# Kernel optimization log

Measured on AMD Instinct MI355X. Metric: run time of the kernel, lower is better.

Reference implementation:

```python
import jax, jax.numpy as jnp
from jax import lax
import numpy as np

N_QUBITS = 8
N_LAYERS = 7
DIM = 2 ** N_QUBITS  # 256 amplitudes


def _conv(x, w, b, stride, pad):
    y = lax.conv_general_dilated(x, w, (stride, stride), [(pad, pad), (pad, pad)],
                                 dimension_numbers=("NCHW", "OIHW", "NCHW"))
    return y + b[None, :, None, None]


def _adaptive_pool2(x):
    # AdaptiveAvgPool2d(2) on 7x7 input: bins [0:4) and [3:7) per spatial dim (overlap at idx 3)
    bins = [(0, 4), (3, 7)]
    rows = [x[:, :, s:e, :].mean(axis=2) for s, e in bins]  # each (B,C,7)
    return jnp.stack([jnp.stack([r[:, :, s:e].mean(axis=2) for s, e in bins], axis=-1)
                      for r in rows], axis=-2)  # (B,C,2,2)


def _qsim(feat, weights):
    # Batched 8-qubit statevector simulation. PennyLane default.qubit ordering:
    # wire 0 is the most-significant axis. RY and CNOT are real matrices and the
    # amplitude-embedded state is real, so the state stays real throughout.
    norm = jnp.linalg.norm(feat, axis=1, keepdims=True)
    state = feat / jnp.maximum(norm, 1e-12)  # AmplitudeEmbedding(normalize=True), (B,256)
    B = state.shape[0]
    for layer in range(N_LAYERS):
        for q in range(N_QUBITS):  # RY(weights[layer,q]) on wire q
            theta = weights[layer, q]
            c, s = jnp.cos(theta / 2), jnp.sin(theta / 2)
            st = state.reshape(B, 2 ** q, 2, 2 ** (N_QUBITS - 1 - q))
            s0, s1 = st[:, :, 0, :], st[:, :, 1, :]
            state = jnp.stack([c * s0 - s * s1, s * s0 + c * s1], axis=2).reshape(B, DIM)
        for q in range(N_QUBITS - 1):  # CNOT(control=q, target=q+1)
            st = state.reshape(B, 2 ** q, 2, 2, 2 ** (N_QUBITS - 2 - q))
            swapped = st[:, :, 1, ::-1, :]  # flip target where control=1
            state = jnp.stack([st[:, :, 0], swapped], axis=2).reshape(B, DIM)
    st = state.reshape(B, 2, DIM // 2)
    return jnp.sum(st[:, 0] ** 2, axis=1) - jnp.sum(st[:, 1] ** 2, axis=1)  # <Z_0>


def setup_inputs() -> dict:
    key = jax.random.key(0)
    ks = jax.random.split(key, 24)
    B = 65536
    f32 = jnp.float32
    def nrm(k, shape, scale):
        return jax.random.normal(k, shape, f32) * scale
    return {
        "x": jax.random.normal(ks[0], (B, 1, 28, 28), f32),
        "conv1_w": nrm(ks[1], (3, 1, 5, 5), 0.2), "conv1_b": nrm(ks[2], (3,), 0.1),
        "conv2_w": nrm(ks[3], (6, 3, 3, 3), 0.2), "conv2_b": nrm(ks[4], (6,), 0.1),
        "conv3_w": nrm(ks[5], (12, 6, 3, 3), 0.2), "conv3_b": nrm(ks[6], (12,), 0.1),
        "fc_w": nrm(ks[7], (256, 48), 0.15), "fc_b": nrm(ks[8], (256,), 0.1),
        "q_weights": jax.random.uniform(ks[9], (N_LAYERS, N_QUBITS), f32, 0.0, 2.0 * np.pi),
        "cls1_w": nrm(ks[10], (180, 1), 0.5), "cls1_b": nrm(ks[11], (180,), 0.1),
        "cls2_w": nrm(ks[12], (140, 180), 0.08), "cls2_b": nrm(ks[13], (140,), 0.1),
        "cls3_w": nrm(ks[14], (100, 140), 0.09), "cls3_b": nrm(ks[15], (100,), 0.1),
        "cls4_w": nrm(ks[16], (50, 100), 0.1), "cls4_b": nrm(ks[17], (50,), 0.1),
        "cls5_w": nrm(ks[18], (1, 50), 0.15), "cls5_b": nrm(ks[19], (1,), 0.1),
    }


def reference(x, conv1_w, conv1_b, conv2_w, conv2_b, conv3_w, conv3_b, fc_w, fc_b,
              q_weights, cls1_w, cls1_b, cls2_w, cls2_b, cls3_w, cls3_b,
              cls4_w, cls4_b, cls5_w, cls5_b):
    h = jax.nn.relu(_conv(x, conv1_w, conv1_b, 2, 2))   # (B,3,14,14)
    h = jax.nn.relu(_conv(h, conv2_w, conv2_b, 2, 1))   # (B,6,7,7)
    h = jax.nn.relu(_conv(h, conv3_w, conv3_b, 1, 1))   # (B,12,7,7)
    h = _adaptive_pool2(h).reshape(h.shape[0], -1)      # (B,48)
    feat = jax.nn.relu(h @ fc_w.T + fc_b)               # (B,256); dropout = identity (eval)
    feat = feat / jnp.maximum(jnp.linalg.norm(feat, axis=1, keepdims=True), 1e-12)  # F.normalize
    qout = _qsim(feat, q_weights)[:, None]              # (B,1)
    h = jax.nn.relu(qout @ cls1_w.T + cls1_b)
    h = jax.nn.relu(h @ cls2_w.T + cls2_b)
    h = jax.nn.relu(h @ cls3_w.T + cls3_b)
    h = jax.nn.relu(h @ cls4_w.T + cls4_b)
    return jax.nn.sigmoid(h @ cls5_w.T + cls5_b)        # (B,1)
```

## Files before the change

### kernel.cpp

```cpp
#include <hip/hip_runtime.h>
#include <math.h>


#define WR2_SZ 1664
#define NL   16384

constexpr int QM[7][8] = {
 {0x80,0x40,0x20,0x10,0x08,0x04,0x02,0x01},
 {0xC0,0x60,0x30,0x18,0x0C,0x06,0x03,0x01},
 {0xA0,0x50,0x28,0x14,0x0A,0x05,0x02,0x01},
 {0xF0,0x78,0x3C,0x1E,0x0F,0x07,0x03,0x01},
 {0x88,0x44,0x22,0x11,0x08,0x04,0x02,0x01},
 {0xCC,0x66,0x33,0x19,0x0C,0x06,0x03,0x01},
 {0xAA,0x55,0x2A,0x15,0x0A,0x05,0x02,0x01}};
constexpr int QR[7][8] = {
 {0x80,0x40,0x20,0x10,0x08,0x04,0x02,0x01},
 {0x80,0xC0,0xE0,0xF0,0xF8,0xFC,0xFE,0xFF},
 {0x80,0x40,0xA0,0x50,0xA8,0x54,0xAA,0x55},
 {0x80,0xC0,0x60,0x30,0x98,0xCC,0x66,0x33},
 {0x80,0x40,0x20,0x10,0x88,0x44,0x22,0x11},
 {0x80,0xC0,0xE0,0xF0,0x78,0x3C,0x1E,0x0F},
 {0x80,0x40,0xA0,0x50,0x28,0x14,0x0A,0x05}};

#define ROTSTEP2(L, Q) { \
    constexpr int m_  = QM[L][Q]; \
    constexpr int r_  = QR[L][Q]; \
    constexpr int lm_ = m_ >> 2, rm_ = m_ & 3; \
    constexpr int rl_ = r_ >> 2, rr_ = r_ & 3; \
    constexpr float f1_ = (rr_ & 1) ? -1.f : 1.f; \
    constexpr float f2_ = (rr_ & 2) ? -1.f : 1.f; \
    constexpr float f3_ = f1_ * f2_; \
    const float c_ = qtc[(L) * 8 + (Q)]; \
    const float s_ = qts[(L) * 8 + (Q)]; \
    float sgn_; \
    if constexpr (rl_ != 0) sgn_ = (__popc(lane & rl_) & 1) ? s_ : -s_; \
    else                    sgn_ = -s_; \
    float2 pU0_ = sU[0 ^ rm_], pU1_ = sU[1 ^ rm_], pU2_ = sU[2 ^ rm_], pU3_ = sU[3 ^ rm_]; \
    float2 pV0_ = sV[0 ^ rm_], pV1_ = sV[1 ^ rm_], pV2_ = sV[2 ^ rm_], pV3_ = sV[3 ^ rm_]; \
    if constexpr (lm_ != 0) { \
        pU0_.x = __shfl_xor(pU0_.x, lm_); pU0_.y = __shfl_xor(pU0_.y, lm_); \
        pU1_.x = __shfl_xor(pU1_.x, lm_); pU1_.y = __shfl_xor(pU1_.y, lm_); \
        pU2_.x = __shfl_xor(pU2_.x, lm_); pU2_.y = __shfl_xor(pU2_.y, lm_); \
        pU3_.x = __shfl_xor(pU3_.x, lm_); pU3_.y = __shfl_xor(pU3_.y, lm_); \
        pV0_.x = __shfl_xor(pV0_.x, lm_); pV0_.y = __shfl_xor(pV0_.y, lm_); \
        pV1_.x = __shfl_xor(pV1_.x, lm_); pV1_.y = __shfl_xor(pV1_.y, lm_); \
        pV2_.x = __shfl_xor(pV2_.x, lm_); pV2_.y = __shfl_xor(pV2_.y, lm_); \
        pV3_.x = __shfl_xor(pV3_.x, lm_); pV3_.y = __shfl_xor(pV3_.y, lm_); \
    } \
    sU[0].x = fmaf(c_, sU[0].x, sgn_ * pU0_.x); \
    sU[0].y = fmaf(c_, sU[0].y, sgn_ * pU0_.y); \
    sU[1].x = fmaf(c_, sU[1].x, (f1_ * sgn_) * pU1_.x); \
    sU[1].y = fmaf(c_, sU[1].y, (f1_ * sgn_) * pU1_.y); \
    sU[2].x = fmaf(c_, sU[2].x, (f2_ * sgn_) * pU2_.x); \
    sU[2].y = fmaf(c_, sU[2].y, (f2_ * sgn_) * pU2_.y); \
    sU[3].x = fmaf(c_, sU[3].x, (f3_ * sgn_) * pU3_.x); \
    sU[3].y = fmaf(c_, sU[3].y, (f3_ * sgn_) * pU3_.y); \
    sV[0].x = fmaf(c_, sV[0].x, sgn_ * pV0_.x); \
    sV[0].y = fmaf(c_, sV[0].y, sgn_ * pV0_.y); \
    sV[1].x = fmaf(c_, sV[1].x, (f1_ * sgn_) * pV1_.x); \
    sV[1].y = fmaf(c_, sV[1].y, (f1_ * sgn_) * pV1_.y); \
    sV[2].x = fmaf(c_, sV[2].x, (f2_ * sgn_) * pV2_.x); \
    sV[2].y = fmaf(c_, sV[2].y, (f2_ * sgn_) * pV2_.y); \
    sV[3].x = fmaf(c_, sV[3].x, (f3_ * sgn_) * pV3_.x); \
    sV[3].y = fmaf(c_, sV[3].y, (f3_ * sgn_) * pV3_.y); \
}

#define ROTLAYER2(L) \
    ROTSTEP2(L,0) ROTSTEP2(L,1) ROTSTEP2(L,2) ROTSTEP2(L,3) \
    ROTSTEP2(L,4) ROTSTEP2(L,5) ROTSTEP2(L,6) ROTSTEP2(L,7)

__global__ __launch_bounds__(256)
void build_lut(const float* __restrict__ w1, const float* __restrict__ b1,
               const float* __restrict__ w2, const float* __restrict__ b2,
               const float* __restrict__ w3, const float* __restrict__ b3,
               const float* __restrict__ w4, const float* __restrict__ b4,
               const float* __restrict__ w5, const float* __restrict__ b5,
               const float* __restrict__ qw,
               float* __restrict__ lut)
{
    __shared__ float hh[16][344];
    const int tid = threadIdx.x;
    const int e = tid >> 4;
    const int w = tid & 15;
    const int idx = blockIdx.x * 16 + e;
    const float t = -1.f + 2.f * (float)idx / (float)(NL - 1);

    if (blockIdx.x == 0 && tid < 56) {
        float th = 0.5f * qw[tid];
        lut[NL + tid]      = cosf(th);
        lut[NL + 56 + tid] = sinf(th);
    }

    float* hA = hh[e];
    float* hB = hA + 184;

    #pragma unroll
    for (int tt = 0; tt < 12; ++tt) {
        int j = tt * 16 + w;
        if (j < 180) hA[j] = fmaxf(fmaf(t, w1[j], b1[j]), 0.f);
    }
    for (int tt = 0; tt < 9; ++tt) {
        int j = tt * 16 + w;
        int jj = (j < 140) ? j : 0;
        const float4* wrow = (const float4*)(w2 + jj * 180);
        float a0 = 0.f, a1 = 0.f, a2 = 0.f, a3 = 0.f;
        for (int kc = 0; kc < 45; ++kc) {
            float4 h4 = *(const float4*)(hA + kc * 4);
            float4 ww = wrow[kc];
            a0 = fmaf(h4.x, ww.x, a0); a1 = fmaf(h4.y, ww.y, a1);
            a2 = fmaf(h4.z, ww.z, a2); a3 = fmaf(h4.w, ww.w, a3);
        }
        if (j < 140) hB[j] = fmaxf((a0 + a1) + (a2 + a3) + b2[j], 0.f);
    }
    for (int tt = 0; tt < 7; ++tt) {
        int j = tt * 16 + w;
        int jj = (j < 100) ? j : 0;
        const float4* wrow = (const float4*)(w3 + jj * 140);
        float a0 = 0.f, a1 = 0.f, a2 = 0.f, a3 = 0.f;
        for (int kc = 0; kc < 35; ++kc) {
            float4 h4 = *(const float4*)(hB + kc * 4);
            float4 ww = wrow[kc];
            a0 = fmaf(h4.x, ww.x, a0); a1 = fmaf(h4.y, ww.y, a1);
            a2 = fmaf(h4.z, ww.z, a2); a3 = fmaf(h4.w, ww.w, a3);
        }
        if (j < 100) hA[j] = fmaxf((a0 + a1) + (a2 + a3) + b3[j], 0.f);
    }
    for (int tt = 0; tt < 4; ++tt) {
        int j = tt * 16 + w;
        int jj = (j < 50) ? j : 0;
        const float4* wrow = (const float4*)(w4 + jj * 100);
        float a0 = 0.f, a1 = 0.f, a2 = 0.f, a3 = 0.f;
        for (int kc = 0; kc < 25; ++kc) {
            float4 h4 = *(const float4*)(hA + kc * 4);
            float4 ww = wrow[kc];
            a0 = fmaf(h4.x, ww.x, a0); a1 = fmaf(h4.y, ww.y, a1);
            a2 = fmaf(h4.z, ww.z, a2); a3 = fmaf(h4.w, ww.w, a3);
        }
        if (j < 50) hB[j] = fmaxf((a0 + a1) + (a2 + a3) + b4[j], 0.f);
    }
    float p5 = 0.f;
    for (int k = w; k < 50; k += 16) p5 = fmaf(hB[k], w5[k], p5);
    #pragma unroll
    for (int m = 1; m < 16; m <<= 1) p5 += __shfl_xor(p5, m);
    if (w == 0) lut[idx] = p5 + b5[0];
}

__global__ __launch_bounds__(256, 3)
void fused_all(const float* __restrict__ x,
               const float* __restrict__ c1w, const float* __restrict__ c1b,
               const float* __restrict__ c2w, const float* __restrict__ c2b,
               const float* __restrict__ c3w, const float* __restrict__ c3b,
               const float* __restrict__ fcw, const float* __restrict__ fcb,
               const float* __restrict__ lut,
               float* __restrict__ out, int B)
{
    __shared__ float2 wreg2[4][WR2_SZ];

    const int tid  = threadIdx.x;
    const int lane = tid & 63;
    const int wv   = tid >> 6;

    const float* qtc = lut + NL;
    const float* qts = lut + NL + 56;

    float2* wr2 = wreg2[wv];
    const int base = blockIdx.x * 16;

    float2* c1p2    = wr2;
    float2* pin2    = wr2 + 672;
    float2* c2pT2   = wr2 + 672;
    float2* c3_2    = wr2;
    float2* pooled2 = wr2 + 600;

    float2 sU[4], sV[4];

    const int o0 = lane * 4;
    const float4* fr0 = (const float4*)(fcw + (o0 + 0) * 48);
    const float4* fr1 = (const float4*)(fcw + (o0 + 1) * 48);
    const float4* fr2 = (const float4*)(fcw + (o0 + 2) * 48);
    const float4* fr3 = (const float4*)(fcw + (o0 + 3) * 48);
    const float4 fb = *(const float4*)(fcb + o0);

    #pragma unroll
    for (int pr = 0; pr < 2; ++pr) {
        int sa = base + wv * 4 + pr * 2;
        sa = (sa < B) ? sa : B - 1;
        const int sb = (sa + 1 < B) ? sa + 1 : sa;

        {
            float4 z4 = {0.f, 0.f, 0.f, 0.f};
            float* w0 = (float*)wr2;
            #pragma unroll
            for (int t = 0; t < 13; ++t)
                *(float4*)(w0 + t * 256 + lane * 4) = z4;
        }
        {
            const float4* xsA = (const float4*)(x + (size_t)sa * 784);
            const float4* xsB = (const float4*)(x + (size_t)sb * 784);
            #pragma unroll
            for (int t = 0; t < 4; ++t) {
                int i4 = t * 64 + lane;
                if (i4 < 196) {
                    float4 va = xsA[i4];
                    float4 vb = xsB[i4];
                    int r = i4 / 7;
                    int c = (i4 % 7) * 4;
                    float2* dst = pin2 + (r + 2) * 32 + (c + 2);
                    dst[0] = make_float2(va.x, vb.x);
                    dst[1] = make_float2(va.y, vb.y);
                    dst[2] = make_float2(va.z, vb.z);
                    dst[3] = make_float2(va.w, vb.w);
                }
            }
        }

        #pragma unroll
        for (int t = 0; t < 4; ++t) {
            int p = t * 64 + lane;
            bool valid = p < 196;
            int pp = valid ? p : 0;
            int y = pp / 14, xx = pp % 14;
            const float2* pr2 = pin2 + (2 * y) * 32 + 2 * xx;
            float2 win[25];
            #pragma unroll
            for (int ky = 0; ky < 5; ++ky) {
                const float2* rw = pr2 + ky * 32;
                #pragma unroll
                for (int j = 0; j < 5; ++j) win[ky * 5 + j] = rw[j];
            }
            #pragma unroll
            for (int c = 0; c < 3; ++c) {
                float ax = c1b[c], ay = c1b[c];
                #pragma unroll
                for (int k = 0; k < 25; ++k) {
                    float wk = c1w[c * 25 + k];
                    ax = fmaf(win[k].x, wk, ax);
                    ay = fmaf(win[k].y, wk, ay);
                }
                if (valid)
                    c1p2[c * 224 + y * 16 + (xx + 1)] =
                        make_float2(fmaxf(ax, 0.f), fmaxf(ay, 0.f));
            }
        }

        {
            float4 z4 = {0.f, 0.f, 0.f, 0.f};
            float4* zz = (float4*)c2pT2;
            #pragma unroll
            for (int t = 0; t < 6; ++t) {
                int i = t * 64 + lane;
                if (i < 324) zz[i] = z4;
            }
        }
        {
            int p = lane;
            bool valid = p < 49;
            int pp = valid ? p : 0;
            int y = pp / 7, xx = pp % 7;
            float acx[6], acy[6];
            #pragma unroll
            for (int c = 0; c < 6; ++c) { acx[c] = c2b[c]; acy[c] = c2b[c]; }
            #pragma unroll
            for (int ic = 0; ic < 3; ++ic) {
                const float2* bic = c1p2 + ic * 224;
                float2 win[9];
                #pragma unroll
                for (int ky = 0; ky < 3; ++ky) {
                    int rr = 2 * y - 1 + ky;
                    bool okr = rr >= 0;
                    int rc = okr ? rr : 0;
                    const float2* rw = bic + rc * 16 + 2 * xx;
                    float2 a0 = rw[0], a1 = rw[1], a2 = rw[2];
                    float2 z2 = {0.f, 0.f};
                    win[ky * 3 + 0] = okr ? a0 : z2;
                    win[ky * 3 + 1] = okr ? a1 : z2;
                    win[ky * 3 + 2] = okr ? a2 : z2;
                }
                #pragma unroll
                for (int c = 0; c < 6; ++c)
                    #pragma unroll
                    for (int k = 0; k < 9; ++k) {
                        float wk = c2w[c * 27 + ic * 9 + k];
                        acx[c] = fmaf(win[k].x, wk, acx[c]);
                        acy[c] = fmaf(win[k].y, wk, acy[c]);
                    }
            }
            if (valid) {
                float2* op = c2pT2 + ((y + 1) * 9 + (xx + 1)) * 8;
                #pragma unroll
                for (int c = 0; c < 6; ++c)
                    op[c] = make_float2(fmaxf(acx[c], 0.f), fmaxf(acy[c], 0.f));
            }
        }

        {
            int p = lane;
            bool valid = p < 49;
            int pp = valid ? p : 0;
            int y = pp / 7, xx = pp % 7;
            float acx[12], acy[12];
            #pragma unroll
            for (int c = 0; c < 12; ++c) { acx[c] = c3b[c]; acy[c] = c3b[c]; }
            #pragma unroll
            for (int dy = 0; dy < 3; ++dy)
                #pragma unroll
                for (int dx = 0; dx < 3; ++dx) {
                    const float2* cp = c2pT2 + ((y + dy) * 9 + (xx + dx)) * 8;
                    float2 ch[6];
                    #pragma unroll
                    for (int j = 0; j < 6; ++j) ch[j] = cp[j];
                    const int k = dy * 3 + dx;
                    #pragma unroll
                    for (int c = 0; c < 12; ++c) {
                        const float* wp = c3w + c * 54 + k;
                        #pragma unroll
                        for (int j = 0; j < 6; ++j) {
                            float wk = wp[j * 9];
                            acx[c] = fmaf(ch[j].x, wk, acx[c]);
                            acy[c] = fmaf(ch[j].y, wk, acy[c]);
                        }
                    }
                }
            if (valid) {
                #pragma unroll
                for (int c = 0; c < 12; ++c)
                    c3_2[c * 49 + p] = make_float2(fmaxf(acx[c], 0.f), fmaxf(acy[c], 0.f));
            }
        }

        {
            int o = lane;
            if (o < 48) {
                int c = o >> 2, i = (o >> 1) & 1, j = o & 1;
                int ri = i * 3, cj = j * 3;
                float sx = 0.f, sy = 0.f;
                #pragma unroll
                for (int dy = 0; dy < 4; ++dy)
                    #pragma unroll
                    for (int dx = 0; dx < 4; ++dx) {
                        float2 v = c3_2[c * 49 + (ri + dy) * 7 + (cj + dx)];
                        sx += v.x; sy += v.y;
                    }
                pooled2[o] = make_float2(sx * (1.f / 16.f), sy * (1.f / 16.f));
            }
        }

        {
            float2 a0 = {0.f, 0.f}, a1 = {0.f, 0.f}, a2 = {0.f, 0.f}, a3 = {0.f, 0.f};
            #pragma unroll
            for (int kc = 0; kc < 12; ++kc) {
                float4 w0 = fr0[kc], w1 = fr1[kc], w2 = fr2[kc], w3 = fr3[kc];
                const float2* pv = pooled2 + kc * 4;
                float2 p0 = pv[0], p1 = pv[1], p2 = pv[2], p3 = pv[3];
                a0.x = fmaf(p0.x, w0.x, fmaf(p1.x, w0.y, fmaf(p2.x, w0.z, fmaf(p3.x, w0.w, a0.x))));
                a0.y = fmaf(p0.y, w0.x, fmaf(p1.y, w0.y, fmaf(p2.y, w0.z, fmaf(p3.y, w0.w, a0.y))));
                a1.x = fmaf(p0.x, w1.x, fmaf(p1.x, w1.y, fmaf(p2.x, w1.z, fmaf(p3.x, w1.w, a1.x))));
                a1.y = fmaf(p0.y, w1.x, fmaf(p1.y, w1.y, fmaf(p2.y, w1.z, fmaf(p3.y, w1.w, a1.y))));
                a2.x = fmaf(p0.x, w2.x, fmaf(p1.x, w2.y, fmaf(p2.x, w2.z, fmaf(p3.x, w2.w, a2.x))));
                a2.y = fmaf(p0.y, w2.x, fmaf(p1.y, w2.y, fmaf(p2.y, w2.z, fmaf(p3.y, w2.w, a2.y))));
                a3.x = fmaf(p0.x, w3.x, fmaf(p1.x, w3.y, fmaf(p2.x, w3.z, fmaf(p3.x, w3.w, a3.x))));
                a3.y = fmaf(p0.y, w3.x, fmaf(p1.y, w3.y, fmaf(p2.y, w3.z, fmaf(p3.y, w3.w, a3.y))));
            }
            float2 t0, t1, t2, t3;
            t0.x = fmaxf(a0.x + fb.x, 0.f); t0.y = fmaxf(a0.y + fb.x, 0.f);
            t1.x = fmaxf(a1.x + fb.y, 0.f); t1.y = fmaxf(a1.y + fb.y, 0.f);
            t2.x = fmaxf(a2.x + fb.z, 0.f); t2.y = fmaxf(a2.y + fb.z, 0.f);
            t3.x = fmaxf(a3.x + fb.w, 0.f); t3.y = fmaxf(a3.y + fb.w, 0.f);
            float ssx = fmaf(t0.x, t0.x, fmaf(t1.x, t1.x, fmaf(t2.x, t2.x, t3.x * t3.x)));
            float ssy = fmaf(t0.y, t0.y, fmaf(t1.y, t1.y, fmaf(t2.y, t2.y, t3.y * t3.y)));
            #pragma unroll
            for (int m = 1; m < 64; m <<= 1) {
                ssx += __shfl_xor(ssx, m);
                ssy += __shfl_xor(ssy, m);
            }
            float scx = 1.f / fmaxf(sqrtf(ssx), 1e-12f);
            float scy = 1.f / fmaxf(sqrtf(ssy), 1e-12f);
            t0.x *= scx; t1.x *= scx; t2.x *= scx; t3.x *= scx;
            t0.y *= scy; t1.y *= scy; t2.y *= scy; t3.y *= scy;
            if (pr == 0) { sU[0] = t0; sU[1] = t1; sU[2] = t2; sU[3] = t3; }
            else         { sV[0] = t0; sV[1] = t1; sV[2] = t2; sV[3] = t3; }
        }
    }

    ROTLAYER2(0) ROTLAYER2(1) ROTLAYER2(2) ROTLAYER2(3)
    ROTLAYER2(4) ROTLAYER2(5) ROTLAYER2(6)

    float2 pU, pV;
    pU.x = sU[0].x*sU[0].x + sU[1].x*sU[1].x + sU[2].x*sU[2].x + sU[3].x*sU[3].x;
    pU.y = sU[0].y*sU[0].y + sU[1].y*sU[1].y + sU[2].y*sU[2].y + sU[3].y*sU[3].y;
    pV.x = sV[0].x*sV[0].x + sV[1].x*sV[1].x + sV[2].x*sV[2].x + sV[3].x*sV[3].x;
    pV.y = sV[0].y*sV[0].y + sV[1].y*sV[1].y + sV[2].y*sV[2].y + sV[3].y*sV[3].y;
    if (lane & 32) { pU.x = -pU.x; pU.y = -pU.y; pV.x = -pV.x; pV.y = -pV.y; }
    #pragma unroll
    for (int m = 1; m < 64; m <<= 1) {
        pU.x += __shfl_xor(pU.x, m); pU.y += __shfl_xor(pU.y, m);
        pV.x += __shfl_xor(pV.x, m); pV.y += __shfl_xor(pV.y, m);
    }

    if (lane < 4) {
        float qout = (lane == 0) ? pU.x : (lane == 1) ? pU.y : (lane == 2) ? pV.x : pV.y;
        int osample = base + wv * 4 + lane;
        float u = (qout + 1.f) * 0.5f * (float)(NL - 1);
        int i0 = (int)floorf(u);
        i0 = (i0 < 0) ? 0 : ((i0 > NL - 2) ? NL - 2 : i0);
        float fr = u - (float)i0;
        float z0 = lut[i0], z1 = lut[i0 + 1];
        float z = fmaf(z1 - z0, fr, z0);
        if (osample < B) out[osample] = 1.f / (1.f + expf(-z));
    }
}

extern "C" void kernel_launch(void* const* d_in, const int* in_sizes, int n_in,
                              void* d_out, int out_size, void* d_ws, size_t ws_size,
                              hipStream_t stream) {
    const float* x   = (const float*)d_in[0];
    const float* c1w = (const float*)d_in[1];
    const float* c1b = (const float*)d_in[2];
    const float* c2w = (const float*)d_in[3];
    const float* c2b = (const float*)d_in[4];
    const float* c3w = (const float*)d_in[5];
    const float* c3b = (const float*)d_in[6];
    const float* fcw = (const float*)d_in[7];
    const float* fcb = (const float*)d_in[8];
    const float* qw  = (const float*)d_in[9];
    const float* w1  = (const float*)d_in[10];
    const float* b1  = (const float*)d_in[11];
    const float* w2  = (const float*)d_in[12];
    const float* b2  = (const float*)d_in[13];
    const float* w3  = (const float*)d_in[14];
    const float* b3  = (const float*)d_in[15];
    const float* w4  = (const float*)d_in[16];
    const float* b4  = (const float*)d_in[17];
    const float* w5  = (const float*)d_in[18];
    const float* b5  = (const float*)d_in[19];

    float* lut = (float*)d_ws;

    int B = in_sizes[0] / 784;

    build_lut<<<dim3(NL / 16), dim3(256), 0, stream>>>(
        w1, b1, w2, b2, w3, b3, w4, b4, w5, b5, qw, lut);

    int grid = (B + 15) / 16;
    fused_all<<<dim3(grid), dim3(256), 0, stream>>>(
        x, c1w, c1b, c2w, c2b, c3w, c3b, fcw, fcb, lut,
        (float*)d_out, B);
}
```

Baseline: 478.4 us.

## Shrink per-wave LDS scratch to raise occupancy to four blocks per CU

Reorganizes the per-wave LDS workspace so that conv1 runs one sample at a time on a scalar padded input buffer, and conv1 output is stored unpadded with left padding handled by predicated loads in conv2. This cuts the per-wave shared buffer from 1664 to 1236 float2, and the launch bounds are raised from 3 to 4 blocks per SM. The aim is higher occupancy to hide latency. In exchange the input is loaded and zeroed twice per pair, conv1 work is split into two passes, and register pressure must fit the tighter bound.

```diff
diff --git a/kernel.cpp b/kernel.cpp
--- a/kernel.cpp
+++ b/kernel.cpp
@@ -2,7 +2,7 @@
 #include <math.h>
 
 
-#define WR2_SZ 1664
+#define WR2_SZ 1236
 #define NL   16384
 
 constexpr int QM[7][8] = {
@@ -145,7 +145,7 @@
     if (w == 0) lut[idx] = p5 + b5[0];
 }
 
-__global__ __launch_bounds__(256, 3)
+__global__ __launch_bounds__(256, 4)
 void fused_all(const float* __restrict__ x,
                const float* __restrict__ c1w, const float* __restrict__ c1b,
                const float* __restrict__ c2w, const float* __restrict__ c2b,
@@ -166,11 +166,12 @@
     float2* wr2 = wreg2[wv];
     const int base = blockIdx.x * 16;
 
-    float2* c1p2    = wr2;
-    float2* pin2    = wr2 + 672;
-    float2* c2pT2   = wr2 + 672;
-    float2* c3_2    = wr2;
-    float2* pooled2 = wr2 + 600;
+    float2* c1p2  = wr2;
+    float2* ovl   = wr2 + 588;
+    float*  pinA  = (float*)ovl;
+    float2* c2pT2 = ovl;
+    float2* c3_2  = wr2;
+    float2* pooled2 = ovl;
 
     float2 sU[4], sV[4];
 
@@ -187,59 +188,62 @@
         sa = (sa < B) ? sa : B - 1;
         const int sb = (sa + 1 < B) ? sa + 1 : sa;
 
-        {
-            float4 z4 = {0.f, 0.f, 0.f, 0.f};
-            float* w0 = (float*)wr2;
-            #pragma unroll
-            for (int t = 0; t < 13; ++t)
-                *(float4*)(w0 + t * 256 + lane * 4) = z4;
-        }
-        {
-            const float4* xsA = (const float4*)(x + (size_t)sa * 784);
-            const float4* xsB = (const float4*)(x + (size_t)sb * 784);
+        #pragma unroll
+        for (int sidx = 0; sidx < 2; ++sidx) {
+            const int s = (sidx == 0) ? sa : sb;
+
+            {
+                float4 z4 = {0.f, 0.f, 0.f, 0.f};
+                float4* pz = (float4*)pinA;
+                #pragma unroll
+                for (int t = 0; t < 4; ++t) {
+                    int i = t * 64 + lane;
+                    if (i < 248) pz[i] = z4;
+                }
+            }
+            {
+                const float4* xs = (const float4*)(x + (size_t)s * 784);
+                #pragma unroll
+                for (int t = 0; t < 4; ++t) {
+                    int i4 = t * 64 + lane;
+                    if (i4 < 196) {
+                        float4 v = xs[i4];
+                        int r = i4 / 7;
+                        int c = (i4 % 7) * 4;
+                        float* dst = pinA + (r + 2) * 32 + (c + 2);
+                        *(float2*)dst       = make_float2(v.x, v.y);
+                        *(float2*)(dst + 2) = make_float2(v.z, v.w);
+                    }
+                }
+            }
             #pragma unroll
             for (int t = 0; t < 4; ++t) {
-                int i4 = t * 64 + lane;
-                if (i4 < 196) {
-                    float4 va = xsA[i4];
-                    float4 vb = xsB[i4];
-                    int r = i4 / 7;
-                    int c = (i4 % 7) * 4;
-                    float2* dst = pin2 + (r + 2) * 32 + (c + 2);
-                    dst[0] = make_float2(va.x, vb.x);
-                    dst[1] = make_float2(va.y, vb.y);
-                    dst[2] = make_float2(va.z, vb.z);
-                    dst[3] = make_float2(va.w, vb.w);
-                }
-            }
-        }
-
-        #pragma unroll
-        for (int t = 0; t < 4; ++t) {
-            int p = t * 64 + lane;
-            bool valid = p < 196;
-            int pp = valid ? p : 0;
-            int y = pp / 14, xx = pp % 14;
-            const float2* pr2 = pin2 + (2 * y) * 32 + 2 * xx;
-            float2 win[25];
-            #pragma unroll
-            for (int ky = 0; ky < 5; ++ky) {
-                const float2* rw = pr2 + ky * 32;
-                #pragma unroll
-                for (int j = 0; j < 5; ++j) win[ky * 5 + j] = rw[j];
-            }
-            #pragma unroll
-            for (int c = 0; c < 3; ++c) {
-                float ax = c1b[c], ay = c1b[c];
-                #pragma unroll
-                for (int k = 0; k < 25; ++k) {
-                    float wk = c1w[c * 25 + k];
-                    ax = fmaf(win[k].x, wk, ax);
-                    ay = fmaf(win[k].y, wk, ay);
-                }
-                if (valid)
-                    c1p2[c * 224 + y * 16 + (xx + 1)] =
-                        make_float2(fmaxf(ax, 0.f), fmaxf(ay, 0.f));
+                int p = t * 64 + lane;
+                bool valid = p < 196;
+                int pp = valid ? p : 0;
+                int y = pp / 14, xx = pp % 14;
+                const float* prw = pinA + (2 * y) * 32 + 2 * xx;
+                float win[25];
+                #pragma unroll
+                for (int ky = 0; ky < 5; ++ky) {
+                    const float* rw = prw + ky * 32;
+                    float2 a = *(const float2*)rw;
+                    float2 b = *(const float2*)(rw + 2);
+                    win[ky * 5 + 0] = a.x; win[ky * 5 + 1] = a.y;
+                    win[ky * 5 + 2] = b.x; win[ky * 5 + 3] = b.y;
+                    win[ky * 5 + 4] = rw[4];
+                }
+                #pragma unroll
+                for (int c = 0; c < 3; ++c) {
+                    float acc = c1b[c];
+                    #pragma unroll
+                    for (int k = 0; k < 25; ++k)
+                        acc = fmaf(win[k], c1w[c * 25 + k], acc);
+                    if (valid) {
+                        float* cf = (float*)&c1p2[c * 196 + y * 14 + xx];
+                        cf[sidx] = fmaxf(acc, 0.f);
+                    }
+                }
             }
         }
 
@@ -257,24 +261,28 @@
             bool valid = p < 49;
             int pp = valid ? p : 0;
             int y = pp / 7, xx = pp % 7;
+            const bool hasL = (xx > 0);
             float acx[6], acy[6];
             #pragma unroll
             for (int c = 0; c < 6; ++c) { acx[c] = c2b[c]; acy[c] = c2b[c]; }
             #pragma unroll
             for (int ic = 0; ic < 3; ++ic) {
-                const float2* bic = c1p2 + ic * 224;
+                const float2* bic = c1p2 + ic * 196;
                 float2 win[9];
+                const float2 z2 = {0.f, 0.f};
                 #pragma unroll
                 for (int ky = 0; ky < 3; ++ky) {
                     int rr = 2 * y - 1 + ky;
                     bool okr = rr >= 0;
                     int rc = okr ? rr : 0;
-                    const float2* rw = bic + rc * 16 + 2 * xx;
-                    float2 a0 = rw[0], a1 = rw[1], a2 = rw[2];
-                    float2 z2 = {0.f, 0.f};
-                    win[ky * 3 + 0] = okr ? a0 : z2;
-                    win[ky * 3 + 1] = okr ? a1 : z2;
-                    win[ky * 3 + 2] = okr ? a2 : z2;
+                    int off = rc * 14 + 2 * xx;
+                    float2 lv = z2;
+                    if (hasL) lv = bic[off - 1];
+                    float2 mv = bic[off];
+                    float2 rv = bic[off + 1];
+                    win[ky * 3 + 0] = okr ? lv : z2;
+                    win[ky * 3 + 1] = okr ? mv : z2;
+                    win[ky * 3 + 2] = okr ? rv : z2;
                 }
                 #pragma unroll
                 for (int c = 0; c < 6; ++c)
```

Result: slower. 912.0 us (+90.6%).

## Interleave qubit rotations of first pair with conv of second pair; zero only borders

Applied to the files above, without the earlier changes.

Each sample pair's statevector rotation is now a separate pass, and the first pair's rotation layers are placed between the conv stages of the second pair, instead of running the conv chain twice and then rotating both states together. The aim is to let LDS-heavy conv work and shuffle-heavy rotation work fill each other's latency within a wave. Full zeroing of the per-wave scratch is replaced by zeroing only the padding borders and column that the convolutions read. The trade-off is that each rotation step now carries half as many independent shuffles, so it exposes more shuffle latency unless the compiler actually mixes the two streams. The border-only zeroing also relies on the exact aliasing layout of the scratch buffers.

```diff
diff --git a/kernel.cpp b/kernel.cpp
--- a/kernel.cpp
+++ b/kernel.cpp
@@ -22,7 +22,7 @@
  {0x80,0xC0,0xE0,0xF0,0x78,0x3C,0x1E,0x0F},
  {0x80,0x40,0xA0,0x50,0x28,0x14,0x0A,0x05}};
 
-#define ROTSTEP2(L, Q) { \
+#define ROTSTEP_S(S, L, Q) { \
     constexpr int m_  = QM[L][Q]; \
     constexpr int r_  = QR[L][Q]; \
     constexpr int lm_ = m_ >> 2, rm_ = m_ & 3; \
@@ -35,39 +35,26 @@
     float sgn_; \
     if constexpr (rl_ != 0) sgn_ = (__popc(lane & rl_) & 1) ? s_ : -s_; \
     else                    sgn_ = -s_; \
-    float2 pU0_ = sU[0 ^ rm_], pU1_ = sU[1 ^ rm_], pU2_ = sU[2 ^ rm_], pU3_ = sU[3 ^ rm_]; \
-    float2 pV0_ = sV[0 ^ rm_], pV1_ = sV[1 ^ rm_], pV2_ = sV[2 ^ rm_], pV3_ = sV[3 ^ rm_]; \
+    float2 p0_ = S[0 ^ rm_], p1_ = S[1 ^ rm_], p2_ = S[2 ^ rm_], p3_ = S[3 ^ rm_]; \
     if constexpr (lm_ != 0) { \
-        pU0_.x = __shfl_xor(pU0_.x, lm_); pU0_.y = __shfl_xor(pU0_.y, lm_); \
-        pU1_.x = __shfl_xor(pU1_.x, lm_); pU1_.y = __shfl_xor(pU1_.y, lm_); \
-        pU2_.x = __shfl_xor(pU2_.x, lm_); pU2_.y = __shfl_xor(pU2_.y, lm_); \
-        pU3_.x = __shfl_xor(pU3_.x, lm_); pU3_.y = __shfl_xor(pU3_.y, lm_); \
-        pV0_.x = __shfl_xor(pV0_.x, lm_); pV0_.y = __shfl_xor(pV0_.y, lm_); \
-        pV1_.x = __shfl_xor(pV1_.x, lm_); pV1_.y = __shfl_xor(pV1_.y, lm_); \
-        pV2_.x = __shfl_xor(pV2_.x, lm_); pV2_.y = __shfl_xor(pV2_.y, lm_); \
-        pV3_.x = __shfl_xor(pV3_.x, lm_); pV3_.y = __shfl_xor(pV3_.y, lm_); \
-    } \
-    sU[0].x = fmaf(c_, sU[0].x, sgn_ * pU0_.x); \
-    sU[0].y = fmaf(c_, sU[0].y, sgn_ * pU0_.y); \
-    sU[1].x = fmaf(c_, sU[1].x, (f1_ * sgn_) * pU1_.x); \
-    sU[1].y = fmaf(c_, sU[1].y, (f1_ * sgn_) * pU1_.y); \
-    sU[2].x = fmaf(c_, sU[2].x, (f2_ * sgn_) * pU2_.x); \
-    sU[2].y = fmaf(c_, sU[2].y, (f2_ * sgn_) * pU2_.y); \
-    sU[3].x = fmaf(c_, sU[3].x, (f3_ * sgn_) * pU3_.x); \
-    sU[3].y = fmaf(c_, sU[3].y, (f3_ * sgn_) * pU3_.y); \
-    sV[0].x = fmaf(c_, sV[0].x, sgn_ * pV0_.x); \
-    sV[0].y = fmaf(c_, sV[0].y, sgn_ * pV0_.y); \
-    sV[1].x = fmaf(c_, sV[1].x, (f1_ * sgn_) * pV1_.x); \
-    sV[1].y = fmaf(c_, sV[1].y, (f1_ * sgn_) * pV1_.y); \
-    sV[2].x = fmaf(c_, sV[2].x, (f2_ * sgn_) * pV2_.x); \
-    sV[2].y = fmaf(c_, sV[2].y, (f2_ * sgn_) * pV2_.y); \
-    sV[3].x = fmaf(c_, sV[3].x, (f3_ * sgn_) * pV3_.x); \
-    sV[3].y = fmaf(c_, sV[3].y, (f3_ * sgn_) * pV3_.y); \
-}
-
-#define ROTLAYER2(L) \
-    ROTSTEP2(L,0) ROTSTEP2(L,1) ROTSTEP2(L,2) ROTSTEP2(L,3) \
-    ROTSTEP2(L,4) ROTSTEP2(L,5) ROTSTEP2(L,6) ROTSTEP2(L,7)
+        p0_.x = __shfl_xor(p0_.x, lm_); p0_.y = __shfl_xor(p0_.y, lm_); \
+        p1_.x = __shfl_xor(p1_.x, lm_); p1_.y = __shfl_xor(p1_.y, lm_); \
+        p2_.x = __shfl_xor(p2_.x, lm_); p2_.y = __shfl_xor(p2_.y, lm_); \
+        p3_.x = __shfl_xor(p3_.x, lm_); p3_.y = __shfl_xor(p3_.y, lm_); \
+    } \
+    S[0].x = fmaf(c_, S[0].x, sgn_ * p0_.x); \
+    S[0].y = fmaf(c_, S[0].y, sgn_ * p0_.y); \
+    S[1].x = fmaf(c_, S[1].x, (f1_ * sgn_) * p1_.x); \
+    S[1].y = fmaf(c_, S[1].y, (f1_ * sgn_) * p1_.y); \
+    S[2].x = fmaf(c_, S[2].x, (f2_ * sgn_) * p2_.x); \
+    S[2].y = fmaf(c_, S[2].y, (f2_ * sgn_) * p2_.y); \
+    S[3].x = fmaf(c_, S[3].x, (f3_ * sgn_) * p3_.x); \
+    S[3].y = fmaf(c_, S[3].y, (f3_ * sgn_) * p3_.y); \
+}
+
+#define ROTLAYER_S(S, L) \
+    ROTSTEP_S(S,L,0) ROTSTEP_S(S,L,1) ROTSTEP_S(S,L,2) ROTSTEP_S(S,L,3) \
+    ROTSTEP_S(S,L,4) ROTSTEP_S(S,L,5) ROTSTEP_S(S,L,6) ROTSTEP_S(S,L,7)
 
 __global__ __launch_bounds__(256)
 void build_lut(const float* __restrict__ w1, const float* __restrict__ b1,
@@ -145,6 +132,226 @@
     if (w == 0) lut[idx] = p5 + b5[0];
 }
 
+
+#define ZERO_PIN_BORDER() { \
+    float4 z4 = {0.f, 0.f, 0.f, 0.f}; \
+    float4* pf = (float4*)pin2; \
+    _Pragma("unroll") \
+    for (int t = 0; t < 2; ++t) { \
+        int i = t * 64 + lane; \
+        if (i < 104) { \
+            int idx_; \
+            if (i < 32) idx_ = i; \
+            else if (i < 48) idx_ = 480 + (i - 32); \
+            else { int k = i - 48; idx_ = (2 + (k >> 1)) * 16 + (k & 1) * 15; } \
+            pf[idx_] = z4; \
+        } \
+    } \
+}
+
+#define ZERO_C1COL0() { \
+    if (lane < 42) { \
+        int c = lane / 14, y = lane % 14; \
+        c1p2[c * 224 + y * 16] = make_float2(0.f, 0.f); \
+    } \
+}
+
+#define ZERO_C2PT_BORDER() { \
+    float4 z4 = {0.f, 0.f, 0.f, 0.f}; \
+    float4* zz = (float4*)c2pT2; \
+    _Pragma("unroll") \
+    for (int t = 0; t < 2; ++t) { \
+        int i = t * 64 + lane; \
+        int b = i >> 2; \
+        int p_; \
+        if (b < 9) p_ = b; \
+        else if (b < 18) p_ = b + 63; \
+        else if (b < 25) p_ = 9 * (b - 17); \
+        else p_ = 9 * (b - 24) + 8; \
+        zz[p_ * 4 + (i & 3)] = z4; \
+    } \
+}
+
+#define STAGE(SA, SB) { \
+    const float4* xsA = (const float4*)(x + (size_t)(SA) * 784); \
+    const float4* xsB = (const float4*)(x + (size_t)(SB) * 784); \
+    _Pragma("unroll") \
+    for (int t = 0; t < 4; ++t) { \
+        int i4 = t * 64 + lane; \
+        if (i4 < 196) { \
+            float4 va = xsA[i4]; \
+            float4 vb = xsB[i4]; \
+            int r = i4 / 7; \
+            int c = (i4 % 7) * 4; \
+            float2* dst = pin2 + (r + 2) * 32 + (c + 2); \
+            dst[0] = make_float2(va.x, vb.x); \
+            dst[1] = make_float2(va.y, vb.y); \
+            dst[2] = make_float2(va.z, vb.z); \
+            dst[3] = make_float2(va.w, vb.w); \
+        } \
+    } \
+}
+
+#define CONV1() { \
+    _Pragma("unroll") \
+    for (int t = 0; t < 4; ++t) { \
+        int p = t * 64 + lane; \
+        bool valid = p < 196; \
+        int pp = valid ? p : 0; \
+        int y = pp / 14, xx = pp % 14; \
+        const float2* pr2 = pin2 + (2 * y) * 32 + 2 * xx; \
+        float2 win[25]; \
+        _Pragma("unroll") \
+        for (int ky = 0; ky < 5; ++ky) { \
+            const float2* rw = pr2 + ky * 32; \
+            _Pragma("unroll") \
+            for (int j = 0; j < 5; ++j) win[ky * 5 + j] = rw[j]; \
+        } \
+        _Pragma("unroll") \
+        for (int c = 0; c < 3; ++c) { \
+            float ax = c1b[c], ay = c1b[c]; \
+            _Pragma("unroll") \
+            for (int k = 0; k < 25; ++k) { \
+                float wk = c1w[c * 25 + k]; \
+                ax = fmaf(win[k].x, wk, ax); \
+                ay = fmaf(win[k].y, wk, ay); \
+            } \
+            if (valid) \
+                c1p2[c * 224 + y * 16 + (xx + 1)] = \
+                    make_float2(fmaxf(ax, 0.f), fmaxf(ay, 0.f)); \
+        } \
+    } \
+}
+
+#define CONV2() { \
+    int p = lane; \
+    bool valid = p < 49; \
+    int pp = valid ? p : 0; \
+    int y = pp / 7, xx = pp % 7; \
+    float acx[6], acy[6]; \
+    _Pragma("unroll") \
+    for (int c = 0; c < 6; ++c) { acx[c] = c2b[c]; acy[c] = c2b[c]; } \
+    _Pragma("unroll") \
+    for (int ic = 0; ic < 3; ++ic) { \
+        const float2* bic = c1p2 + ic * 224; \
+        float2 win[9]; \
+        const float2 z2 = {0.f, 0.f}; \
+        _Pragma("unroll") \
+        for (int ky = 0; ky < 3; ++ky) { \
+            int rr = 2 * y - 1 + ky; \
+            bool okr = rr >= 0; \
+            int rc = okr ? rr : 0; \
+            const float2* rw = bic + rc * 16 + 2 * xx; \
+            float2 a0w = rw[0], a1w = rw[1], a2w = rw[2]; \
+            win[ky * 3 + 0] = okr ? a0w : z2; \
+            win[ky * 3 + 1] = okr ? a1w : z2; \
+            win[ky * 3 + 2] = okr ? a2w : z2; \
+        } \
+        _Pragma("unroll") \
+        for (int c = 0; c < 6; ++c) \
+            _Pragma("unroll") \
+            for (int k = 0; k < 9; ++k) { \
+                float wk = c2w[c * 27 + ic * 9 + k]; \
+                acx[c] = fmaf(win[k].x, wk, acx[c]); \
+                acy[c] = fmaf(win[k].y, wk, acy[c]); \
+            } \
+    } \
+    if (valid) { \
+        float2* op = c2pT2 + ((y + 1) * 9 + (xx + 1)) * 8; \
+        _Pragma("unroll") \
+        for (int c = 0; c < 6; ++c) \
+            op[c] = make_float2(fmaxf(acx[c], 0.f), fmaxf(acy[c], 0.f)); \
+    } \
+}
+
+#define CONV3() { \
+    int p = lane; \
+    bool valid = p < 49; \
+    int pp = valid ? p : 0; \
+    int y = pp / 7, xx = pp % 7; \
+    float acx[12], acy[12]; \
+    _Pragma("unroll") \
+    for (int c = 0; c < 12; ++c) { acx[c] = c3b[c]; acy[c] = c3b[c]; } \
+    _Pragma("unroll") \
+    for (int dy = 0; dy < 3; ++dy) \
+        _Pragma("unroll") \
+        for (int dx = 0; dx < 3; ++dx) { \
+            const float2* cp = c2pT2 + ((y + dy) * 9 + (xx + dx)) * 8; \
+            float2 ch[6]; \
+            _Pragma("unroll") \
+            for (int j = 0; j < 6; ++j) ch[j] = cp[j]; \
+            const int k = dy * 3 + dx; \
+            _Pragma("unroll") \
+            for (int c = 0; c < 12; ++c) { \
+                const float* wp = c3w + c * 54 + k; \
+                _Pragma("unroll") \
+                for (int j = 0; j < 6; ++j) { \
+                    float wk = wp[j * 9]; \
+                    acx[c] = fmaf(ch[j].x, wk, acx[c]); \
+                    acy[c] = fmaf(ch[j].y, wk, acy[c]); \
+                } \
+            } \
+        } \
+    if (valid) { \
+        _Pragma("unroll") \
+        for (int c = 0; c < 12; ++c) \
+            c3_2[c * 49 + p] = make_float2(fmaxf(acx[c], 0.f), fmaxf(acy[c], 0.f)); \
+    } \
+}
+
+#define POOL() { \
+    int o = lane; \
+    if (o < 48) { \
+        int c = o >> 2, i = (o >> 1) & 1, j = o & 1; \
+        int ri = i * 3, cj = j * 3; \
+        float sx = 0.f, sy = 0.f; \
+        _Pragma("unroll") \
+        for (int dy = 0; dy < 4; ++dy) \
+            _Pragma("unroll") \
+            for (int dx = 0; dx < 4; ++dx) { \
+                float2 v = c3_2[c * 49 + (ri + dy) * 7 + (cj + dx)]; \
+                sx += v.x; sy += v.y; \
+            } \
+        pooled2[o] = make_float2(sx * (1.f / 16.f), sy * (1.f / 16.f)); \
+    } \
+}
+
+#define FC_NORM(SDST) { \
+    float2 a0 = {0.f,0.f}, a1 = {0.f,0.f}, a2 = {0.f,0.f}, a3 = {0.f,0.f}; \
+    _Pragma("unroll") \
+    for (int kc = 0; kc < 12; ++kc) { \
+        float4 w0 = fr0[kc], w1 = fr1[kc], w2 = fr2[kc], w3 = fr3[kc]; \
+        const float2* pv = pooled2 + kc * 4; \
+        float2 p0 = pv[0], p1 = pv[1], p2 = pv[2], p3 = pv[3]; \
+        a0.x = fmaf(p0.x, w0.x, fmaf(p1.x, w0.y, fmaf(p2.x, w0.z, fmaf(p3.x, w0.w, a0.x)))); \
+        a0.y = fmaf(p0.y, w0.x, fmaf(p1.y, w0.y, fmaf(p2.y, w0.z, fmaf(p3.y, w0.w, a0.y)))); \
+        a1.x = fmaf(p0.x, w1.x, fmaf(p1.x, w1.y, fmaf(p2.x, w1.z, fmaf(p3.x, w1.w, a1.x)))); \
+        a1.y = fmaf(p0.y, w1.x, fmaf(p1.y, w1.y, fmaf(p2.y, w1.z, fmaf(p3.y, w1.w, a1.y)))); \
+        a2.x = fmaf(p0.x, w2.x, fmaf(p1.x, w2.y, fmaf(p2.x, w2.z, fmaf(p3.x, w2.w, a2.x)))); \
+        a2.y = fmaf(p0.y, w2.x, fmaf(p1.y, w2.y, fmaf(p2.y, w2.z, fmaf(p3.y, w2.w, a2.y)))); \
+        a3.x = fmaf(p0.x, w3.x, fmaf(p1.x, w3.y, fmaf(p2.x, w3.z, fmaf(p3.x, w3.w, a3.x)))); \
+        a3.y = fmaf(p0.y, w3.x, fmaf(p1.y, w3.y, fmaf(p2.y, w3.z, fmaf(p3.y, w3.w, a3.y)))); \
+    } \
+    float2 t0, t1, t2, t3; \
+    t0.x = fmaxf(a0.x + fb.x, 0.f); t0.y = fmaxf(a0.y + fb.x, 0.f); \
+    t1.x = fmaxf(a1.x + fb.y, 0.f); t1.y = fmaxf(a1.y + fb.y, 0.f); \
+    t2.x = fmaxf(a2.x + fb.z, 0.f); t2.y = fmaxf(a2.y + fb.z, 0.f); \
+    t3.x = fmaxf(a3.x + fb.w, 0.f); t3.y = fmaxf(a3.y + fb.w, 0.f); \
+    float ssx = fmaf(t0.x, t0.x, fmaf(t1.x, t1.x, fmaf(t2.x, t2.x, t3.x * t3.x))); \
+    float ssy = fmaf(t0.y, t0.y, fmaf(t1.y, t1.y, fmaf(t2.y, t2.y, t3.y * t3.y))); \
+    _Pragma("unroll") \
+    for (int m = 1; m < 64; m <<= 1) { \
+        ssx += __shfl_xor(ssx, m); \
+        ssy += __shfl_xor(ssy, m); \
+    } \
+    float scx = 1.f / fmaxf(sqrtf(ssx), 1e-12f); \
+    float scy = 1.f / fmaxf(sqrtf(ssy), 1e-12f); \
+    SDST[0] = make_float2(t0.x * scx, t0.y * scy); \
+    SDST[1] = make_float2(t1.x * scx, t1.y * scy); \
+    SDST[2] = make_float2(t2.x * scx, t2.y * scy); \
+    SDST[3] = make_float2(t3.x * scx, t3.y * scy); \
+}
+
 __global__ __launch_bounds__(256, 3)
 void fused_all(const float* __restrict__ x,
                const float* __restrict__ c1w, const float* __restrict__ c1b,
@@ -181,209 +388,55 @@
     const float4* fr3 = (const float4*)(fcw + (o0 + 3) * 48);
     const float4 fb = *(const float4*)(fcb + o0);
 
-    #pragma unroll
-    for (int pr = 0; pr < 2; ++pr) {
-        int sa = base + wv * 4 + pr * 2;
-        sa = (sa < B) ? sa : B - 1;
-        const int sb = (sa + 1 < B) ? sa + 1 : sa;
-
-        {
-            float4 z4 = {0.f, 0.f, 0.f, 0.f};
-            float* w0 = (float*)wr2;
-            #pragma unroll
-            for (int t = 0; t < 13; ++t)
-                *(float4*)(w0 + t * 256 + lane * 4) = z4;
-        }
-        {
-            const float4* xsA = (const float4*)(x + (size_t)sa * 784);
-            const float4* xsB = (const float4*)(x + (size_t)sb * 784);
-            #pragma unroll
-            for (int t = 0; t < 4; ++t) {
-                int i4 = t * 64 + lane;
-                if (i4 < 196) {
-                    float4 va = xsA[i4];
-                    float4 vb = xsB[i4];
-                    int r = i4 / 7;
-                    int c = (i4 % 7) * 4;
-                    float2* dst = pin2 + (r + 2) * 32 + (c + 2);
-                    dst[0] = make_float2(va.x, vb.x);
-                    dst[1] = make_float2(va.y, vb.y);
-                    dst[2] = make_float2(va.z, vb.z);
-                    dst[3] = make_float2(va.w, vb.w);
-                }
-            }
-        }
-
-        #pragma unroll
-        for (int t = 0; t < 4; ++t) {
-            int p = t * 64 + lane;
-            bool valid = p < 196;
-            int pp = valid ? p : 0;
-            int y = pp / 14, xx = pp % 14;
-            const float2* pr2 = pin2 + (2 * y) * 32 + 2 * xx;
-            float2 win[25];
-            #pragma unroll
-            for (int ky = 0; ky < 5; ++ky) {
-                const float2* rw = pr2 + ky * 32;
-                #pragma unroll
-                for (int j = 0; j < 5; ++j) win[ky * 5 + j] = rw[j];
-            }
-            #pragma unroll
-            for (int c = 0; c < 3; ++c) {
-                float ax = c1b[c], ay = c1b[c];
-                #pragma unroll
-                for (int k = 0; k < 25; ++k) {
-                    float wk = c1w[c * 25 + k];
-                    ax = fmaf(win[k].x, wk, ax);
-                    ay = fmaf(win[k].y, wk, ay);
-                }
-                if (valid)
-                    c1p2[c * 224 + y * 16 + (xx + 1)] =
-                        make_float2(fmaxf(ax, 0.f), fmaxf(ay, 0.f));
-            }
-        }
-
-        {
-            float4 z4 = {0.f, 0.f, 0.f, 0.f};
-            float4* zz = (float4*)c2pT2;
-            #pragma unroll
-            for (int t = 0; t < 6; ++t) {
-                int i = t * 64 + lane;
-                if (i < 324) zz[i] = z4;
-            }
-        }
-        {
-            int p = lane;
-            bool valid = p < 49;
-            int pp = valid ? p : 0;
-            int y = pp / 7, xx = pp % 7;
-            float acx[6], acy[6];
-            #pragma unroll
-            for (int c = 0; c < 6; ++c) { acx[c] = c2b[c]; acy[c] = c2b[c]; }
-            #pragma unroll
-            for (int ic = 0; ic < 3; ++ic) {
-                const float2* bic = c1p2 + ic * 224;
-                float2 win[9];
-                #pragma unroll
-                for (int ky = 0; ky < 3; ++ky) {
-                    int rr = 2 * y - 1 + ky;
-                    bool okr = rr >= 0;
-                    int rc = okr ? rr : 0;
-                    const float2* rw = bic + rc * 16 + 2 * xx;
-                    float2 a0 = rw[0], a1 = rw[1], a2 = rw[2];
-                    float2 z2 = {0.f, 0.f};
-                    win[ky * 3 + 0] = okr ? a0 : z2;
-                    win[ky * 3 + 1] = okr ? a1 : z2;
-                    win[ky * 3 + 2] = okr ? a2 : z2;
-                }
-                #pragma unroll
-                for (int c = 0; c < 6; ++c)
-                    #pragma unroll
-                    for (int k = 0; k < 9; ++k) {
-                        float wk = c2w[c * 27 + ic * 9 + k];
-                        acx[c] = fmaf(win[k].x, wk, acx[c]);
-                        acy[c] = fmaf(win[k].y, wk, acy[c]);
-                    }
-            }
-            if (valid) {
-                float2* op = c2pT2 + ((y + 1) * 9 + (xx + 1)) * 8;
-                #pragma unroll
-                for (int c = 0; c < 6; ++c)
-                    op[c] = make_float2(fmaxf(acx[c], 0.f), fmaxf(acy[c], 0.f));
-            }
-        }
-
-        {
-            int p = lane;
-            bool valid = p < 49;
-            int pp = valid ? p : 0;
-            int y = pp / 7, xx = pp % 7;
-            float acx[12], acy[12];
-            #pragma unroll
-            for (int c = 0; c < 12; ++c) { acx[c] = c3b[c]; acy[c] = c3b[c]; }
-            #pragma unroll
-            for (int dy = 0; dy < 3; ++dy)
-                #pragma unroll
-                for (int dx = 0; dx < 3; ++dx) {
-                    const float2* cp = c2pT2 + ((y + dy) * 9 + (xx + dx)) * 8;
-                    float2 ch[6];
-                    #pragma unroll
-                    for (int j = 0; j < 6; ++j) ch[j] = cp[j];
-                    const int k = dy * 3 + dx;
-                    #pragma unroll
-                    for (int c = 0; c < 12; ++c) {
-                        const float* wp = c3w + c * 54 + k;
-                        #pragma unroll
-                        for (int j = 0; j < 6; ++j) {
-                            float wk = wp[j * 9];
-                            acx[c] = fmaf(ch[j].x, wk, acx[c]);
-                            acy[c] = fmaf(ch[j].y, wk, acy[c]);
-                        }
-                    }
-                }
-            if (valid) {
-                #pragma unroll
-                for (int c = 0; c < 12; ++c)
-                    c3_2[c * 49 + p] = make_float2(fmaxf(acx[c], 0.f), fmaxf(acy[c], 0.f));
-            }
-        }
-
-        {
-            int o = lane;
-            if (o < 48) {
-                int c = o >> 2, i = (o >> 1) & 1, j = o & 1;
-                int ri = i * 3, cj = j * 3;
-                float sx = 0.f, sy = 0.f;
-                #pragma unroll
-                for (int dy = 0; dy < 4; ++dy)
-                    #pragma unroll
-                    for (int dx = 0; dx < 4; ++dx) {
-                        float2 v = c3_2[c * 49 + (ri + dy) * 7 + (cj + dx)];
-                        sx += v.x; sy += v.y;
-                    }
-                pooled2[o] = make_float2(sx * (1.f / 16.f), sy * (1.f / 16.f));
-            }
-        }
-
-        {
-            float2 a0 = {0.f, 0.f}, a1 = {0.f, 0.f}, a2 = {0.f, 0.f}, a3 = {0.f, 0.f};
-            #pragma unroll
-            for (int kc = 0; kc < 12; ++kc) {
-                float4 w0 = fr0[kc], w1 = fr1[kc], w2 = fr2[kc], w3 = fr3[kc];
-                const float2* pv = pooled2 + kc * 4;
-                float2 p0 = pv[0], p1 = pv[1], p2 = pv[2], p3 = pv[3];
-                a0.x = fmaf(p0.x, w0.x, fmaf(p1.x, w0.y, fmaf(p2.x, w0.z, fmaf(p3.x, w0.w, a0.x))));
-                a0.y = fmaf(p0.y, w0.x, fmaf(p1.y, w0.y, fmaf(p2.y, w0.z, fmaf(p3.y, w0.w, a0.y))));
-                a1.x = fmaf(p0.x, w1.x, fmaf(p1.x, w1.y, fmaf(p2.x, w1.z, fmaf(p3.x, w1.w, a1.x))));
-                a1.y = fmaf(p0.y, w1.x, fmaf(p1.y, w1.y, fmaf(p2.y, w1.z, fmaf(p3.y, w1.w, a1.y))));
-                a2.x = fmaf(p0.x, w2.x, fmaf(p1.x, w2.y, fmaf(p2.x, w2.z, fmaf(p3.x, w2.w, a2.x))));
-                a2.y = fmaf(p0.y, w2.x, fmaf(p1.y, w2.y, fmaf(p2.y, w2.z, fmaf(p3.y, w2.w, a2.y))));
-                a3.x = fmaf(p0.x, w3.x, fmaf(p1.x, w3.y, fmaf(p2.x, w3.z, fmaf(p3.x, w3.w, a3.x))));
-                a3.y = fmaf(p0.y, w3.x, fmaf(p1.y, w3.y, fmaf(p2.y, w3.z, fmaf(p3.y, w3.w, a3.y))));
-            }
-            float2 t0, t1, t2, t3;
-            t0.x = fmaxf(a0.x + fb.x, 0.f); t0.y = fmaxf(a0.y + fb.x, 0.f);
-            t1.x = fmaxf(a1.x + fb.y, 0.f); t1.y = fmaxf(a1.y + fb.y, 0.f);
-            t2.x = fmaxf(a2.x + fb.z, 0.f); t2.y = fmaxf(a2.y + fb.z, 0.f);
-            t3.x = fmaxf(a3.x + fb.w, 0.f); t3.y = fmaxf(a3.y + fb.w, 0.f);
-            float ssx = fmaf(t0.x, t0.x, fmaf(t1.x, t1.x, fmaf(t2.x, t2.x, t3.x * t3.x)));
-            float ssy = fmaf(t0.y, t0.y, fmaf(t1.y, t1.y, fmaf(t2.y, t2.y, t3.y * t3.y)));
-            #pragma unroll
-            for (int m = 1; m < 64; m <<= 1) {
-                ssx += __shfl_xor(ssx, m);
-                ssy += __shfl_xor(ssy, m);
-            }
-            float scx = 1.f / fmaxf(sqrtf(ssx), 1e-12f);
-            float scy = 1.f / fmaxf(sqrtf(ssy), 1e-12f);
-            t0.x *= scx; t1.x *= scx; t2.x *= scx; t3.x *= scx;
-            t0.y *= scy; t1.y *= scy; t2.y *= scy; t3.y *= scy;
-            if (pr == 0) { sU[0] = t0; sU[1] = t1; sU[2] = t2; sU[3] = t3; }
-            else         { sV[0] = t0; sV[1] = t1; sV[2] = t2; sV[3] = t3; }
-        }
-    }
-
-    ROTLAYER2(0) ROTLAYER2(1) ROTLAYER2(2) ROTLAYER2(3)
-    ROTLAYER2(4) ROTLAYER2(5) ROTLAYER2(6)
+    int sa0 = base + wv * 4;
+    sa0 = (sa0 < B) ? sa0 : B - 1;
+    const int sb0 = (sa0 + 1 < B) ? sa0 + 1 : sa0;
+    int sa1 = base + wv * 4 + 2;
+    sa1 = (sa1 < B) ? sa1 : B - 1;
+    const int sb1 = (sa1 + 1 < B) ? sa1 + 1 : sa1;
+
+    ZERO_PIN_BORDER();
+    ZERO_C1COL0();
+    STAGE(sa0, sb0);
+    CONV1();
+    ZERO_C2PT_BORDER();
+    CONV2();
+    CONV3();
+
+    ZERO_PIN_BORDER();
+    STAGE(sa1, sb1);
+
+    POOL();
+    FC_NORM(sU);
+
+    ZERO_C1COL0();
+
+    ROTLAYER_S(sU, 0)
+    ROTLAYER_S(sU, 1)
+
+    CONV1();
+
+    ROTLAYER_S(sU, 2)
+    ROTLAYER_S(sU, 3)
+    ROTLAYER_S(sU, 4)
+
+    ZERO_C2PT_BORDER();
+    CONV2();
+
+    ROTLAYER_S(sU, 5)
+    ROTLAYER_S(sU, 6)
+
+    CONV3();
+    POOL();
+    FC_NORM(sV);
+
+    ROTLAYER_S(sV, 0)
+    ROTLAYER_S(sV, 1)
+    ROTLAYER_S(sV, 2)
+    ROTLAYER_S(sV, 3)
+    ROTLAYER_S(sV, 4)
+    ROTLAYER_S(sV, 5)
+    ROTLAYER_S(sV, 6)
 
     float2 pU, pV;
     pU.x = sU[0].x*sU[0].x + sU[1].x*sU[1].x + sU[2].x*sU[2].x + sU[3].x*sU[3].x;
```

Result: slower. 643.0 us (+34.4%).
